# Optimization experiments

Hardware: AMD Instinct MI355X
Metric: run time of the kernel (lower is better)

The kernel has to match this reference:

```python
import jax, jax.numpy as jnp
import numpy as np

B, S, D, H = 2, 2048, 1024, 16
DK = D // H

def setup_inputs() -> dict:
    key = jax.random.key(0)
    k1, k2, k3 = jax.random.split(key, 3)
    std = 2.0 / (D + 3 * D)
    x = jax.random.normal(k1, (B, S, D), dtype=jnp.float32)
    W_qkv = jax.random.normal(k2, (3 * D, D), dtype=jnp.float32) * std
    W_out = jax.random.normal(k3, (D, D), dtype=jnp.float32) * (2.0 / (2 * D))
    return {"x": x, "W_qkv": W_qkv, "W_out": W_out}

def reference(x, W_qkv, W_out):
    # fused QKV projection: [..., d_in] x [d_out, d_in] -> [..., d_out]
    proj = jnp.einsum('bsd,ed->bse', x, W_qkv)               # [B,S,3*H*DK]
    proj = proj.reshape(B, S, 3, H, DK)
    q = proj[:, :, 0].transpose(0, 2, 1, 3)                  # [B,H,S,DK]
    k = proj[:, :, 1].transpose(0, 2, 1, 3)
    v = proj[:, :, 2].transpose(0, 2, 1, 3)
    scores = jnp.einsum('bhnd,bhmd->bhnm', q, k) / jnp.sqrt(jnp.float32(DK))
    causal = jnp.tril(jnp.ones((S, S), dtype=bool))
    scores = jnp.where(causal, scores, -jnp.inf)
    attn = jax.nn.softmax(scores, axis=-1)
    out = jnp.einsum('bhnm,bhmd->bhnd', attn, v)             # [B,H,S,DK]
    out = out.transpose(0, 2, 1, 3).reshape(B, S, H * DK)
    return jnp.einsum('bsd,ed->bse', out, W_out)             # [B,S,D]
```

## Files before the change

kernel.cpp:

```cpp
#include <hip/hip_runtime.h>
#include <hip/hip_bf16.h>
#include <stdint.h>

typedef __attribute__((ext_vector_type(8)))  __bf16 bf16x8;
typedef __attribute__((ext_vector_type(8)))  short  short8;
typedef __attribute__((ext_vector_type(4)))  float  f32x4;
typedef __attribute__((ext_vector_type(16))) float  f32x16;

#define MFMA16(a, b, c) __builtin_amdgcn_mfma_f32_16x16x32_bf16((a), (b), (c), 0, 0, 0)
#define MFMA32(a, b, c) __builtin_amdgcn_mfma_f32_32x32x16_bf16((a), (b), (c), 0, 0, 0)

__device__ __forceinline__ unsigned short f32_bf16(float f) {
  union { float f; unsigned u; } v; v.f = f;
  unsigned r = v.u + 0x7FFFu + ((v.u >> 16) & 1u);
  return (unsigned short)(r >> 16);
}

__device__ __forceinline__ float fast_exp2(float x) {
#if __has_builtin(__builtin_amdgcn_exp2f)
  return __builtin_amdgcn_exp2f(x);
#else
  return __expf(x * 0.69314718f);
#endif
}

__device__ __forceinline__ void gload16(const unsigned short* g, unsigned short* l) {
  __builtin_amdgcn_global_load_lds(
      (const __attribute__((address_space(1))) unsigned int*)(g),
      (__attribute__((address_space(3))) unsigned int*)(l), 16, 0, 0);
}

__global__ void cvt3_kernel(const float* __restrict__ a, int na4,
                            const float* __restrict__ b, int nb4,
                            const float* __restrict__ c, int nc4,
                            unsigned short* __restrict__ oa,
                            unsigned short* __restrict__ ob,
                            unsigned short* __restrict__ oc) {
  int total = na4 + nb4 + nc4;
  for (int i = blockIdx.x * blockDim.x + threadIdx.x; i < total; i += gridDim.x * blockDim.x) {
    const float* src; unsigned short* dst; int j = i;
    if (j < na4) { src = a; dst = oa; }
    else if (j - na4 < nb4) { j -= na4; src = b; dst = ob; }
    else { j -= na4 + nb4; src = c; dst = oc; }
    float4 v = reinterpret_cast<const float4*>(src)[j];
    ushort4 o4;
    o4.x = f32_bf16(v.x); o4.y = f32_bf16(v.y);
    o4.z = f32_bf16(v.z); o4.w = f32_bf16(v.w);
    reinterpret_cast<ushort4*>(dst)[j] = o4;
  }
}

__global__ __launch_bounds__(512, 2) void gemm_qkv_8ph(const unsigned short* __restrict__ A,
                                                       const unsigned short* __restrict__ Bm,
                                                       unsigned short* __restrict__ qkv) {
  extern __shared__ unsigned short SM[];
  const int tid  = threadIdx.x;
  const int lane = tid & 63;
  const int w    = tid >> 6;
  const int wr   = w >> 2, wc = w & 3;
  const int l16  = lane & 15, lh = lane >> 4;
  const int sw   = l16 & 7;
  const int m0   = blockIdx.y * 256;
  const int n0   = blockIdx.x * 256;

  f32x4 acc[8][4];
#pragma unroll
  for (int mi = 0; mi < 8; ++mi)
#pragma unroll
    for (int ni = 0; ni < 4; ++ni) acc[mi][ni] = 0.f;

  const int r0 = tid >> 3,         h0 = (tid & 7) ^ (r0 & 7);
  const int r1 = (tid + 512) >> 3, h1 = (tid & 7) ^ (r1 & 7);
  const unsigned short* Asrc[2][2];
  const unsigned short* Bsrc[2][2];
  Asrc[0][0] = A + (size_t)(m0 + r0) * 1024 + h0 * 8;
  Asrc[0][1] = A + (size_t)(m0 + r1) * 1024 + h1 * 8;
  Asrc[1][0] = A + (size_t)(m0 + 128 + r0) * 1024 + h0 * 8;
  Asrc[1][1] = A + (size_t)(m0 + 128 + r1) * 1024 + h1 * 8;
  Bsrc[0][0] = Bm + (size_t)(n0 + r0) * 1024 + h0 * 8;
  Bsrc[0][1] = Bm + (size_t)(n0 + r1) * 1024 + h1 * 8;
  Bsrc[1][0] = Bm + (size_t)(n0 + 128 + r0) * 1024 + h0 * 8;
  Bsrc[1][1] = Bm + (size_t)(n0 + 128 + r1) * 1024 + h1 * 8;
  const int ld0 = (w * 64) * 8;
  const int ld1 = (512 + w * 64) * 8;

#define STAGE_A(buf, h, U) do { \
    gload16(Asrc[h][0] + (U) * 64, SM + (buf) * 32768 + (h) * 8192 + ld0); \
    gload16(Asrc[h][1] + (U) * 64, SM + (buf) * 32768 + (h) * 8192 + ld1); } while (0)
#define STAGE_B(buf, h, U) do { \
    gload16(Bsrc[h][0] + (U) * 64, SM + (buf) * 32768 + 16384 + (h) * 8192 + ld0); \
    gload16(Bsrc[h][1] + (U) * 64, SM + (buf) * 32768 + 16384 + (h) * 8192 + ld1); } while (0)

  STAGE_A(0, 0, 0); STAGE_A(0, 1, 0);
  STAGE_B(0, 0, 0); STAGE_B(0, 1, 0);
  STAGE_B(1, 0, 1); STAGE_B(1, 1, 1);
  asm volatile("s_waitcnt vmcnt(4)" ::: "memory");
  __builtin_amdgcn_s_barrier();

  const int NT = 16;
#pragma unroll 2
  for (int U = 0; U < NT; ++U) {
    const int b = U & 1;
    const unsigned short* Ab = SM + b * 32768 + wr * 8192;
    const unsigned short* Bb = SM + b * 32768 + 16384 + (wc >> 1) * 8192;
    const int rB = (wc & 1) * 64;
    bf16x8 bfr[4][2], af[2][2];

#define LDA(i, j) (*(const bf16x8*)(Ab + (((i) * 16 + l16) * 8 + (((j) * 4 + lh) ^ sw)) * 8))
#define LDB(n, j) (*(const bf16x8*)(Bb + (((rB + (n) * 16 + l16)) * 8 + (((j) * 4 + lh) ^ sw)) * 8))
#define PHASE_MFMA(p) \
    __builtin_amdgcn_s_setprio(1); \
    _Pragma("unroll") \
    for (int n = 0; n < 4; ++n) { \
      acc[2*(p)][n]   = MFMA16(af[0][0], bfr[n][0], acc[2*(p)][n]); \
      acc[2*(p)][n]   = MFMA16(af[0][1], bfr[n][1], acc[2*(p)][n]); \
      acc[2*(p)+1][n] = MFMA16(af[1][0], bfr[n][0], acc[2*(p)+1][n]); \
      acc[2*(p)+1][n] = MFMA16(af[1][1], bfr[n][1], acc[2*(p)+1][n]); \
    } \
    __builtin_amdgcn_s_setprio(0);

    af[0][0] = LDA(0, 0); af[0][1] = LDA(0, 1);
    af[1][0] = LDA(1, 0); af[1][1] = LDA(1, 1);
#pragma unroll
    for (int n = 0; n < 4; ++n) { bfr[n][0] = LDB(n, 0); bfr[n][1] = LDB(n, 1); }
    if (U + 1 < NT) STAGE_A(b ^ 1, 0, U + 1);
    __builtin_amdgcn_s_barrier();
    PHASE_MFMA(0)
    __builtin_amdgcn_s_barrier();
    af[0][0] = LDA(2, 0); af[0][1] = LDA(2, 1);
    af[1][0] = LDA(3, 0); af[1][1] = LDA(3, 1);
    if (U + 1 < NT) STAGE_A(b ^ 1, 1, U + 1);
    __builtin_amdgcn_s_barrier();
    PHASE_MFMA(1)
    __builtin_amdgcn_s_barrier();
    af[0][0] = LDA(4, 0); af[0][1] = LDA(4, 1);
    af[1][0] = LDA(5, 0); af[1][1] = LDA(5, 1);
    if (U + 2 < NT) STAGE_B(b, 0, U + 2);
    __builtin_amdgcn_s_barrier();
    PHASE_MFMA(2)
    __builtin_amdgcn_s_barrier();
    af[0][0] = LDA(6, 0); af[0][1] = LDA(6, 1);
    af[1][0] = LDA(7, 0); af[1][1] = LDA(7, 1);
    if (U + 2 < NT) STAGE_B(b, 1, U + 2);
    __builtin_amdgcn_s_barrier();
    PHASE_MFMA(3)
    asm volatile("s_waitcnt vmcnt(4)" ::: "memory");
    __builtin_amdgcn_s_barrier();
#undef LDA
#undef LDB
#undef PHASE_MFMA
  }

  __syncthreads();
  unsigned short* Ep = SM + w * 8192;
  const int gn0 = n0 + wc * 64;
  const int cc  = gn0 >> 10;
  const int hh2 = (gn0 & 1023) >> 6;
  const int gm0 = m0 + wr * 128;
  const int bb2 = gm0 >> 11;
  const int ss0 = gm0 & 2047;
  const int bh2 = bb2 * 16 + hh2;

  if (cc < 2) {
    const float qsc = (cc == 0) ? 0.18033688f : 1.0f;
#pragma unroll
    for (int mi = 0; mi < 8; ++mi)
#pragma unroll
      for (int ni = 0; ni < 4; ++ni)
#pragma unroll
        for (int r = 0; r < 4; ++r) {
          int row = mi * 16 + lh * 4 + r;
          int col = (ni * 16 + l16) ^ (lh << 3);
          Ep[row * 64 + col] = f32_bf16(acc[mi][ni][r] * qsc);
        }
    unsigned short* qk = qkv + (((size_t)cc * 32 + bh2) * 2048 + ss0) * 64;
#pragma unroll
    for (int it = 0; it < 16; ++it) {
      int ci = it * 64 + lane;
      int row = ci >> 3, c = ci & 7;
      short8 vv = *(const short8*)(Ep + row * 64 + ((c ^ ((row >> 2) & 3)) * 8));
      *(short8*)(qk + (size_t)row * 64 + c * 8) = vv;
    }
  } else {
#pragma unroll
    for (int mi = 0; mi < 8; ++mi)
#pragma unroll
      for (int ni = 0; ni < 4; ++ni) {
        int dk = ni * 16 + l16;
        int ssl = mi * 16 + lh * 4;
        unsigned lo, hi;
        asm("v_cvt_pk_bf16_f32 %0, %1, %2" : "=v"(lo) : "v"(acc[mi][ni][0]), "v"(acc[mi][ni][1]));
        asm("v_cvt_pk_bf16_f32 %0, %1, %2" : "=v"(hi) : "v"(acc[mi][ni][2]), "v"(acc[mi][ni][3]));
        int off = dk * 128 + (ssl ^ ((dk & 7) << 3));
        *(uint2*)(Ep + off) = make_uint2(lo, hi);
      }
    unsigned short* vt = qkv + (size_t)8388608 + (size_t)bh2 * 64 * 2048 + ss0;
#pragma unroll
    for (int it = 0; it < 16; ++it) {
      int ci = it * 64 + lane;
      int dk = ci >> 4, c = ci & 15;
      short8 vv = *(const short8*)(Ep + dk * 128 + ((c ^ (dk & 7)) * 8));
      *(short8*)(vt + (size_t)dk * 2048 + c * 8) = vv;
    }
  }
#undef STAGE_A
#undef STAGE_B
}

__global__ __launch_bounds__(256) void gemm_out(const unsigned short* __restrict__ A,
                                                const unsigned short* __restrict__ Bm,
                                                float* __restrict__ C,
                                                int M, int N, int K) {
  extern __shared__ unsigned short SM[];
  unsigned short* As = SM;
  unsigned short* Bs = SM + 4096;
  const int tid  = threadIdx.x;
  const int lane = tid & 63;
  const int wid  = tid >> 6;
  const int wr   = wid >> 1, wc = wid & 1;
  const int l16  = lane & 15, lh = lane >> 4;
  const int m0   = blockIdx.y * 128;
  const int n0   = blockIdx.x * 128;

  f32x4 acc[4][4];
#pragma unroll
  for (int mi = 0; mi < 4; ++mi)
#pragma unroll
    for (int ni = 0; ni < 4; ++ni) acc[mi][ni] = 0.f;

  const int c0 = tid, c1 = 256 + tid;
  const unsigned short* a0 = A + (size_t)(m0 + (c0 >> 2)) * K + (c0 & 3) * 8;
  const unsigned short* a1 = A + (size_t)(m0 + (c1 >> 2)) * K + (c1 & 3) * 8;
  const unsigned short* b0 = Bm + (size_t)(n0 + (c0 >> 2)) * K + (c0 & 3) * 8;
  const unsigned short* b1 = Bm + (size_t)(n0 + (c1 >> 2)) * K + (c1 & 3) * 8;
  const int d0 = wid * 64 * 8;
  const int d1 = (256 + wid * 64) * 8;

  for (int k0 = 0; k0 < K; k0 += 32) {
    __syncthreads();
    gload16(a0 + k0, As + d0);
    gload16(a1 + k0, As + d1);
    gload16(b0 + k0, Bs + d0);
    gload16(b1 + k0, Bs + d1);
    __syncthreads();
    bf16x8 af[4], bfr[4];
#pragma unroll
    for (int i = 0; i < 4; ++i) {
      af[i]  = *(const bf16x8*)(As + (wr * 64 + i * 16 + l16) * 32 + lh * 8);
      bfr[i] = *(const bf16x8*)(Bs + (wc * 64 + i * 16 + l16) * 32 + lh * 8);
    }
#pragma unroll
    for (int mi = 0; mi < 4; ++mi)
#pragma unroll
      for (int ni = 0; ni < 4; ++ni)
        acc[mi][ni] = MFMA16(af[mi], bfr[ni], acc[mi][ni]);
  }

  __syncthreads();
  float* Ef = (float*)(SM + wid * 4096);
  const int gm0 = m0 + wr * 64;
  const int gn0 = n0 + wc * 64;
#pragma unroll
  for (int p = 0; p < 2; ++p) {
#pragma unroll
    for (int mi = 0; mi < 4; ++mi)
#pragma unroll
      for (int q = 0; q < 2; ++q) {
        int ni = 2 * p + q;
#pragma unroll
        for (int r = 0; r < 4; ++r) {
          int row = mi * 16 + lh * 4 + r;
          int col = (q * 16 + l16) ^ ((row & 7) << 2);
          Ef[row * 32 + col] = acc[mi][ni][r];
        }
      }
#pragma unroll
    for (int it = 0; it < 8; ++it) {
      int ci = it * 64 + lane;
      int row = ci >> 3, c4 = ci & 7;
      float4 vv = *(const float4*)(Ef + row * 32 + ((c4 * 4) ^ ((row & 7) << 2)));
      *(float4*)(&C[(size_t)(gm0 + row) * N + gn0 + p * 32 + c4 * 4]) = vv;
    }
  }
}

__device__ const signed char JQT[48] = {31,31,30,15, 30,29,29,28,14, 28,27,27,26,13, 26,25,25,24,12,
                                        24,23,23,22,11, 22,21,21,20,10, 20,19,19,18, 9, 18,17,17,16, 8,
                                        16, 7, 6, 5, 4, 3, 2, 1, 0};
__device__ const signed char JS0[48] = { 0,16, 0, 0, 16, 0,15, 0, 0, 15, 0,14, 0, 0, 14, 0,13, 0, 0,
                                        13, 0,12, 0, 0, 12, 0,11, 0, 0, 11, 0,10, 0, 0, 10, 0, 9, 0, 0,
                                         9, 0, 0, 0, 0, 0, 0, 0, 0};
__device__ const signed char JNT[48] = {16,16,16,16, 15,15,15,15,15, 14,14,14,14,14, 13,13,13,13,13,
                                        12,12,12,12,12, 11,11,11,11,11, 10,10,10,10,10,  9, 9, 9, 9, 9,
                                         8, 8, 7, 6, 5, 4, 3, 2, 1};
__device__ const signed char JSL[48] = {30,31,28,-1, 29,26,27,24,-1, 25,22,23,20,-1, 21,18,19,16,-1,
                                        17,14,15,12,-1, 13,10,11, 8,-1,  9, 6, 7, 4,-1,  5, 2, 3, 0,-1,
                                         1,-1,-1,-1,-1,-1,-1,-1,-1};

__global__ __launch_bounds__(256) void attn_kernel(const unsigned short* __restrict__ Qg,
                                                   const unsigned short* __restrict__ Kg,
                                                   const unsigned short* __restrict__ Vtg,
                                                   unsigned short* __restrict__ Og,
                                                   char* __restrict__ parts) {
  __shared__ unsigned short Ks[2][64 * 64];
  __shared__ unsigned short Vs[2][64 * 64];

  const int tid  = threadIdx.x;
  const int lane = tid & 63;
  const int w    = tid >> 6;
  const int wq   = w & 1, wkv = w >> 1;
  const int l31  = lane & 31, hi = lane >> 5;
  const int rx0  = (l31 ^ (l31 >> 3)) & 7;

  const int jb   = blockIdx.x >> 5;
  const int bh   = blockIdx.x & 31;
  const int qt   = JQT[jb];
  const int ts0  = JS0[jb];
  const int tend = ts0 + JNT[jb];
  const int slot = JSL[jb];
  const int bb   = bh >> 4, hh = bh & 15;
  const int qb   = qt * 64;
  const int qcol = qb + wq * 32 + l31;

  const unsigned short* Qh = Qg + (size_t)bh * (2048 * 64);
  const unsigned short* Kh = Kg + (size_t)bh * (2048 * 64);
  const unsigned short* Vh = Vtg + (size_t)bh * (64 * 2048);

  bf16x8 qf[4];
#pragma unroll
  for (int ks = 0; ks < 4; ++ks)
    qf[ks] = *(const bf16x8*)(Qh + (size_t)qcol * 64 + ks * 16 + hi * 8);

  f32x16 o0 = 0.f, o1 = 0.f;
  float mreg = 0.f, ll = 0.f;

  const int sA = tid, sB = tid + 256;
  const int rA = sA >> 3, hA = (sA & 7) ^ ((rA ^ (rA >> 3)) & 7);
  const int rB = sB >> 3, hB = (sB & 7) ^ ((rB ^ (rB >> 3)) & 7);
  const unsigned short* kSrcA = Kh + rA * 64 + hA * 8;
  const unsigned short* kSrcB = Kh + rB * 64 + hB * 8;
  const unsigned short* vSrcA = Vh + (size_t)rA * 2048 + hA * 8;
  const unsigned short* vSrcB = Vh + (size_t)rB * 2048 + hB * 8;
  const int ldsA = (w * 64) * 8;
  const int ldsB = (256 + w * 64) * 8;

  gload16(kSrcA + (size_t)(ts0 * 64) * 64, &Ks[0][ldsA]);
  gload16(kSrcB + (size_t)(ts0 * 64) * 64, &Ks[0][ldsB]);
  gload16(vSrcA + ts0 * 64, &Vs[0][ldsA]);
  gload16(vSrcB + ts0 * 64, &Vs[0][ldsB]);
  __syncthreads();

  const unsigned short* kA = kSrcA + (size_t)(ts0 + 1) * 4096;
  const unsigned short* kB = kSrcB + (size_t)(ts0 + 1) * 4096;
  const unsigned short* vA = vSrcA + (ts0 + 1) * 64;
  const unsigned short* vB = vSrcB + (ts0 + 1) * 64;

  for (int t = ts0; t < tend; ++t) {
    const int kv0 = t * 64;
    const int cur = (t - ts0) & 1;
    if (t + 1 < tend) {
      gload16(kA, &Ks[cur ^ 1][ldsA]);
      gload16(kB, &Ks[cur ^ 1][ldsB]);
      gload16(vA, &Vs[cur ^ 1][ldsA]);
      gload16(vB, &Vs[cur ^ 1][ldsB]);
      kA += 4096; kB += 4096; vA += 64; vB += 64;
    }
    const unsigned short* Kb = Ks[cur];
    const unsigned short* Vb = Vs[cur];

    f32x16 s = 0.f;
    const int kvl = wkv * 32 + l31;
#pragma unroll
    for (int ks = 0; ks < 4; ++ks) {
      int c = (ks * 2 + hi) ^ rx0 ^ (wkv << 2);
      bf16x8 ka = *(const bf16x8*)(Kb + kvl * 64 + c * 8);
      s = MFMA32(ka, qf[ks], s);
    }

    if (t == qt) {
#pragma unroll
      for (int r = 0; r < 16; ++r) {
        int kvp = kv0 + wkv * 32 + (r & 3) + 8 * (r >> 2) + 4 * hi;
        if (kvp > qcol) s[r] = -__builtin_inff();
      }
    }

    float pm = fmaxf(fmaxf(s[0], s[1]), s[2]);
    pm = fmaxf(fmaxf(pm, s[3]), s[4]);
    pm = fmaxf(fmaxf(pm, s[5]), s[6]);
    pm = fmaxf(fmaxf(pm, s[7]), s[8]);
    pm = fmaxf(fmaxf(pm, s[9]), s[10]);
    pm = fmaxf(fmaxf(pm, s[11]), s[12]);
    pm = fmaxf(fmaxf(pm, s[13]), s[14]);
    pm = fmaxf(pm, s[15]);
    if (!__all(pm <= mreg + 8.f)) {
      float t0 = fmaxf(pm, __shfl_xor(pm, 32));
      float mn = fmaxf(mreg, t0);
      float esc = fast_exp2(mreg - mn);
      mreg = mn; ll *= esc;
#pragma unroll
      for (int r = 0; r < 16; ++r) { o0[r] *= esc; o1[r] *= esc; }
    }

    float p[16];
#pragma unroll
    for (int r = 0; r < 16; ++r) p[r] = fast_exp2(s[r] - mreg);
    float ps = ((p[0] + p[1]) + (p[2] + p[3])) + ((p[4] + p[5]) + (p[6] + p[7]))
             + ((p[8] + p[9]) + (p[10] + p[11])) + ((p[12] + p[13]) + (p[14] + p[15]));
    ps += __shfl_xor(ps, 32);
    ll += ps;

    bf16x8 pf[2];
#pragma unroll
    for (int ks = 0; ks < 2; ++ks) {
      const int off = ks * 8;
      unsigned a1, b1, a2, b2;
      asm("v_cvt_pk_bf16_f32 %0, %1, %2" : "=v"(a1) : "v"(p[off + 0]), "v"(p[off + 1]));
      asm("v_cvt_pk_bf16_f32 %0, %1, %2" : "=v"(b1) : "v"(p[off + 4]), "v"(p[off + 5]));
      asm("v_cvt_pk_bf16_f32 %0, %1, %2" : "=v"(a2) : "v"(p[off + 2]), "v"(p[off + 3]));
      asm("v_cvt_pk_bf16_f32 %0, %1, %2" : "=v"(b2) : "v"(p[off + 6]), "v"(p[off + 7]));
      asm("v_permlane32_swap_b32 %0, %1" : "+v"(a1), "+v"(b1));
      asm("v_permlane32_swap_b32 %0, %1" : "+v"(a2), "+v"(b2));
      union { unsigned u[4]; bf16x8 f; } fr;
      fr.u[0] = a1; fr.u[1] = a2; fr.u[2] = b1; fr.u[3] = b2;
      pf[ks] = fr.f;
    }

#pragma unroll
    for (int ks = 0; ks < 2; ++ks) {
      int cbase = wkv * 4 + ks * 2 + hi;
      bf16x8 va0 = *(const bf16x8*)(Vb + l31 * 64 + (cbase ^ rx0) * 8);
      bf16x8 va1 = *(const bf16x8*)(Vb + (32 + l31) * 64 + (cbase ^ rx0 ^ 4) * 8);
      o0 = MFMA32(va0, pf[ks], o0);
      o1 = MFMA32(va1, pf[ks], o1);
    }
    __syncthreads();
  }

  float* oxch = (float*)Ks;
  float* lmx  = (float*)Vs;
  if (wkv == 1) {
    float* dst = oxch + wq * 2048;
#pragma unroll
    for (int r = 0; r < 16; ++r) {
      int d0 = (r & 3) + 8 * (r >> 2) + 4 * hi;
      dst[d0 * 32 + l31] = o0[r];
      dst[(32 + d0) * 32 + l31] = o1[r];
    }
    if (hi == 0) { lmx[wq * 64 + l31] = ll; lmx[wq * 64 + 32 + l31] = mreg; }
  }
  __syncthreads();
  if (wkv == 0) {
    float lB = lmx[wq * 64 + l31];
    float mB = lmx[wq * 64 + 32 + l31];
    float mx = fmaxf(mreg, mB);
    float wA = fast_exp2(mreg - mx), wB = fast_exp2(mB - mx);
    float lT = ll * wA + lB * wB;
    float inv = (slot < 0) ? (1.f / lT) : 1.f;
    float sA2 = wA * inv, sB2 = wB * inv;
    const float* src = oxch + wq * 2048;
    unsigned short* slab = (unsigned short*)((char*)Vs + 1024) + wq * 2048;
#pragma unroll
    for (int i = 0; i < 8; ++i) {
      int r = 2 * i;
      int d0 = (r & 3) + 8 * (r >> 2) + 4 * hi;
      float x0 = o0[r] * sA2 + src[d0 * 32 + l31] * sB2;
      float x1 = o0[r + 1] * sA2 + src[(d0 + 1) * 32 + l31] * sB2;
      float y0 = o1[r] * sA2 + src[(32 + d0) * 32 + l31] * sB2;
      float y1 = o1[r + 1] * sA2 + src[(33 + d0) * 32 + l31] * sB2;
      unsigned u0, u1;
      asm("v_cvt_pk_bf16_f32 %0, %1, %2" : "=v"(u0) : "v"(x0), "v"(x1));
      asm("v_cvt_pk_bf16_f32 %0, %1, %2" : "=v"(u1) : "v"(y0), "v"(y1));
      *(unsigned*)(slab + l31 * 64 + (((d0 >> 3) ^ (l31 & 7)) * 8) + (d0 & 7)) = u0;
      int d1 = 32 + d0;
      *(unsigned*)(slab + l31 * 64 + (((d1 >> 3) ^ (l31 & 7)) * 8) + (d1 & 7)) = u1;
    }
    if (slot < 0) {
      unsigned short* op = Og + (size_t)bb * 2048 * 1024 + (size_t)hh * 64;
#pragma unroll
      for (int it = 0; it < 4; ++it) {
        int ci = it * 64 + lane;
        int qr = ci >> 3, c = ci & 7;
        short8 vv = *(const short8*)(slab + qr * 64 + ((c ^ (qr & 7)) * 8));
        *(short8*)(op + (size_t)(qb + wq * 32 + qr) * 1024 + c * 8) = vv;
      }
    } else {
      char* pb = parts + (size_t)(bh * 32 + slot) * 8704;
      float* pl = (float*)pb;
      float* pmv = pl + 64;
      unsigned short* pO = (unsigned short*)(pb + 512);
      if (hi == 0) { pl[wq * 32 + l31] = lT; pmv[wq * 32 + l31] = mx; }
#pragma unroll
      for (int it = 0; it < 4; ++it) {
        int ci = it * 64 + lane;
        int qr = ci >> 3, c = ci & 7;
        short8 vv = *(const short8*)(slab + qr * 64 + ((c ^ (qr & 7)) * 8));
        *(short8*)(pO + (size_t)(wq * 32 + qr) * 64 + c * 8) = vv;
      }
    }
  }
}

__global__ __launch_bounds__(256) void merge_kernel(const char* __restrict__ parts,
                                                    unsigned short* __restrict__ Og) {
  const int task = blockIdx.x;
  const int bh = task & 31, qi = task >> 5;
  const int qt = 16 + qi;
  const int bb = bh >> 4, hh = bh & 15;
  const int tid = threadIdx.x;
  const int r = tid >> 2, q = tid & 3;

  const char* pb1 = parts + (size_t)(bh * 32 + 2 * qi) * 8704;
  const char* pb2 = parts + (size_t)(bh * 32 + 2 * qi + 1) * 8704;
  const float* l1p = (const float*)pb1;
  const float* l2p = (const float*)pb2;
  float lv1 = l1p[r], mv1 = l1p[64 + r];
  float lv2 = l2p[r], mv2 = l2p[64 + r];
  float mx = fmaxf(mv1, mv2);
  float w1 = fast_exp2(mv1 - mx), w2 = fast_exp2(mv2 - mx);
  float inv = 1.f / (lv1 * w1 + lv2 * w2);
  float s1 = w1 * inv, s2 = w2 * inv;

  const unsigned short* O1 = (const unsigned short*)(pb1 + 512) + r * 64 + q * 16;
  const unsigned short* O2 = (const unsigned short*)(pb2 + 512) + r * 64 + q * 16;
  short8 a0 = *(const short8*)(O1);
  short8 a1 = *(const short8*)(O1 + 8);
  short8 b0 = *(const short8*)(O2);
  short8 b1 = *(const short8*)(O2 + 8);

  unsigned outw[8];
#pragma unroll
  for (int i = 0; i < 4; ++i) {
    float x0 = __builtin_bit_cast(float, ((unsigned)(unsigned short)a0[2 * i]) << 16) * s1 +
               __builtin_bit_cast(float, ((unsigned)(unsigned short)b0[2 * i]) << 16) * s2;
    float x1 = __builtin_bit_cast(float, ((unsigned)(unsigned short)a0[2 * i + 1]) << 16) * s1 +
               __builtin_bit_cast(float, ((unsigned)(unsigned short)b0[2 * i + 1]) << 16) * s2;
    asm("v_cvt_pk_bf16_f32 %0, %1, %2" : "=v"(outw[i]) : "v"(x0), "v"(x1));
    float y0 = __builtin_bit_cast(float, ((unsigned)(unsigned short)a1[2 * i]) << 16) * s1 +
               __builtin_bit_cast(float, ((unsigned)(unsigned short)b1[2 * i]) << 16) * s2;
    float y1 = __builtin_bit_cast(float, ((unsigned)(unsigned short)a1[2 * i + 1]) << 16) * s1 +
               __builtin_bit_cast(float, ((unsigned)(unsigned short)b1[2 * i + 1]) << 16) * s2;
    asm("v_cvt_pk_bf16_f32 %0, %1, %2" : "=v"(outw[4 + i]) : "v"(y0), "v"(y1));
  }
  unsigned short* op = Og + ((size_t)bb * 2048 + qt * 64 + r) * 1024 + hh * 64 + q * 16;
  *(uint4*)(op)     = make_uint4(outw[0], outw[1], outw[2], outw[3]);
  *(uint4*)(op + 8) = make_uint4(outw[4], outw[5], outw[6], outw[7]);
}

extern "C" void kernel_launch(void* const* d_in, const int* in_sizes, int n_in,
                              void* d_out, int out_size, void* d_ws, size_t ws_size,
                              hipStream_t stream) {
  const float* x    = (const float*)d_in[0];
  const float* Wqkv = (const float*)d_in[1];
  const float* Wout = (const float*)d_in[2];
  float* out = (float*)d_out;

  char* ws = (char*)d_ws;
  unsigned short* xb  = (unsigned short*)(ws);
  unsigned short* wqb = (unsigned short*)(ws + (size_t)8 * 1024 * 1024);
  unsigned short* wob = (unsigned short*)(ws + (size_t)14 * 1024 * 1024);
  unsigned short* qkv = (unsigned short*)(ws + (size_t)16 * 1024 * 1024);
  unsigned short* att = (unsigned short*)(ws + (size_t)40 * 1024 * 1024);
  char* parts = ws;

  static bool attr_set = false;
  if (!attr_set) {
    hipFuncSetAttribute((const void*)gemm_qkv_8ph,
                        hipFuncAttributeMaxDynamicSharedMemorySize, 131072);
    attr_set = true;
  }

  cvt3_kernel<<<2048, 256, 0, stream>>>(x, 4194304 / 4, Wqkv, 3145728 / 4,
                                        Wout, 1048576 / 4, xb, wqb, wob);

  gemm_qkv_8ph<<<dim3(12, 16), 512, 131072, stream>>>(xb, wqb, qkv);

  const unsigned short* Qp  = qkv;
  const unsigned short* Kp  = qkv + 4194304;
  const unsigned short* Vtp = qkv + 8388608;
  attn_kernel<<<1536, 256, 0, stream>>>(Qp, Kp, Vtp, att, parts);
  merge_kernel<<<512, 256, 0, stream>>>(parts, att);

  gemm_out<<<dim3(8, 32), 256, 32768, stream>>>(att, wob, out, 4096, 1024, 1024);
}
```

Before: 112.5 us.

## Shrink output GEMM tile to 64x128 and compute softmax row sums via MFMA

The output projection GEMM now uses 64x128 tiles with each wave owning a 64x32 slice, doubling the grid to 512 blocks to fill more CUs at the cost of lower per-block operand reuse. In the attention kernel, the per-row softmax denominator is no longer built from scalar adds plus a cross-lane shuffle. It is accumulated by two extra MFMAs that multiply an all-ones matrix by the bf16 probability fragments, so the sum is taken over bf16-rounded probabilities and adds matrix-core work in exchange for fewer VALU ops.

```diff
diff --git a/kernel.cpp b/kernel.cpp
--- a/kernel.cpp
+++ b/kernel.cpp
@@ -213,74 +213,65 @@
                                                 int M, int N, int K) {
   extern __shared__ unsigned short SM[];
   unsigned short* As = SM;
-  unsigned short* Bs = SM + 4096;
+  unsigned short* Bs = SM + 2048;
   const int tid  = threadIdx.x;
   const int lane = tid & 63;
   const int wid  = tid >> 6;
-  const int wr   = wid >> 1, wc = wid & 1;
   const int l16  = lane & 15, lh = lane >> 4;
-  const int m0   = blockIdx.y * 128;
+  const int m0   = blockIdx.y * 64;
   const int n0   = blockIdx.x * 128;
 
-  f32x4 acc[4][4];
+  f32x4 acc[4][2];
 #pragma unroll
   for (int mi = 0; mi < 4; ++mi)
 #pragma unroll
-    for (int ni = 0; ni < 4; ++ni) acc[mi][ni] = 0.f;
-
-  const int c0 = tid, c1 = 256 + tid;
-  const unsigned short* a0 = A + (size_t)(m0 + (c0 >> 2)) * K + (c0 & 3) * 8;
-  const unsigned short* a1 = A + (size_t)(m0 + (c1 >> 2)) * K + (c1 & 3) * 8;
-  const unsigned short* b0 = Bm + (size_t)(n0 + (c0 >> 2)) * K + (c0 & 3) * 8;
-  const unsigned short* b1 = Bm + (size_t)(n0 + (c1 >> 2)) * K + (c1 & 3) * 8;
-  const int d0 = wid * 64 * 8;
-  const int d1 = (256 + wid * 64) * 8;
+    for (int ni = 0; ni < 2; ++ni) acc[mi][ni] = 0.f;
+
+  const unsigned short* aSrc = A + (size_t)(m0 + (tid >> 2)) * K + (tid & 3) * 8;
+  const unsigned short* b0   = Bm + (size_t)(n0 + (tid >> 2)) * K + (tid & 3) * 8;
+  const unsigned short* b1   = Bm + (size_t)(n0 + 64 + (tid >> 2)) * K + (tid & 3) * 8;
+  const int dA  = wid * 512;
+  const int dB0 = wid * 512;
+  const int dB1 = 2048 + wid * 512;
 
   for (int k0 = 0; k0 < K; k0 += 32) {
     __syncthreads();
-    gload16(a0 + k0, As + d0);
-    gload16(a1 + k0, As + d1);
-    gload16(b0 + k0, Bs + d0);
-    gload16(b1 + k0, Bs + d1);
+    gload16(aSrc + k0, As + dA);
+    gload16(b0 + k0, Bs + dB0);
+    gload16(b1 + k0, Bs + dB1);
     __syncthreads();
-    bf16x8 af[4], bfr[4];
-#pragma unroll
-    for (int i = 0; i < 4; ++i) {
-      af[i]  = *(const bf16x8*)(As + (wr * 64 + i * 16 + l16) * 32 + lh * 8);
-      bfr[i] = *(const bf16x8*)(Bs + (wc * 64 + i * 16 + l16) * 32 + lh * 8);
-    }
+    bf16x8 af[4], bfr[2];
 #pragma unroll
     for (int mi = 0; mi < 4; ++mi)
-#pragma unroll
-      for (int ni = 0; ni < 4; ++ni)
+      af[mi] = *(const bf16x8*)(As + (mi * 16 + l16) * 32 + lh * 8);
+#pragma unroll
+    for (int ni = 0; ni < 2; ++ni)
+      bfr[ni] = *(const bf16x8*)(Bs + (wid * 32 + ni * 16 + l16) * 32 + lh * 8);
+#pragma unroll
+    for (int mi = 0; mi < 4; ++mi)
+#pragma unroll
+      for (int ni = 0; ni < 2; ++ni)
         acc[mi][ni] = MFMA16(af[mi], bfr[ni], acc[mi][ni]);
   }
 
   __syncthreads();
-  float* Ef = (float*)(SM + wid * 4096);
-  const int gm0 = m0 + wr * 64;
-  const int gn0 = n0 + wc * 64;
-#pragma unroll
-  for (int p = 0; p < 2; ++p) {
-#pragma unroll
-    for (int mi = 0; mi < 4; ++mi)
-#pragma unroll
-      for (int q = 0; q < 2; ++q) {
-        int ni = 2 * p + q;
-#pragma unroll
-        for (int r = 0; r < 4; ++r) {
-          int row = mi * 16 + lh * 4 + r;
-          int col = (q * 16 + l16) ^ ((row & 7) << 2);
-          Ef[row * 32 + col] = acc[mi][ni][r];
-        }
+  float* Ef = (float*)SM + wid * 2048;
+#pragma unroll
+  for (int mi = 0; mi < 4; ++mi)
+#pragma unroll
+    for (int ni = 0; ni < 2; ++ni)
+#pragma unroll
+      for (int r = 0; r < 4; ++r) {
+        int row = mi * 16 + lh * 4 + r;
+        int col = (ni * 16 + l16) ^ ((row & 7) << 2);
+        Ef[row * 32 + col] = acc[mi][ni][r];
       }
 #pragma unroll
-    for (int it = 0; it < 8; ++it) {
-      int ci = it * 64 + lane;
-      int row = ci >> 3, c4 = ci & 7;
-      float4 vv = *(const float4*)(Ef + row * 32 + ((c4 * 4) ^ ((row & 7) << 2)));
-      *(float4*)(&C[(size_t)(gm0 + row) * N + gn0 + p * 32 + c4 * 4]) = vv;
-    }
+  for (int it = 0; it < 8; ++it) {
+    int ci = it * 64 + lane;
+    int row = ci >> 3, c4 = ci & 7;
+    float4 vv = *(const float4*)(Ef + row * 32 + ((c4 * 4) ^ ((row & 7) << 2)));
+    *(float4*)(&C[(size_t)(m0 + row) * N + n0 + wid * 32 + c4 * 4]) = vv;
   }
 }
 
@@ -331,8 +322,14 @@
   for (int ks = 0; ks < 4; ++ks)
     qf[ks] = *(const bf16x8*)(Qh + (size_t)qcol * 64 + ks * 16 + hi * 8);
 
+  union { short8 s; bf16x8 b; } oneu;
+#pragma unroll
+  for (int j = 0; j < 8; ++j) oneu.s[j] = 0x3F80;
+  const bf16x8 onesf = oneu.b;
+
   f32x16 o0 = 0.f, o1 = 0.f;
-  float mreg = 0.f, ll = 0.f;
+  f32x16 o_l = 0.f;
+  float mreg = 0.f;
 
   const int sA = tid, sB = tid + 256;
   const int rA = sA >> 3, hA = (sA & 7) ^ ((rA ^ (rA >> 3)) & 7);
@@ -397,7 +394,8 @@
       float t0 = fmaxf(pm, __shfl_xor(pm, 32));
       float mn = fmaxf(mreg, t0);
       float esc = fast_exp2(mreg - mn);
-      mreg = mn; ll *= esc;
+      mreg = mn;
+      o_l[0] *= esc;
 #pragma unroll
       for (int r = 0; r < 16; ++r) { o0[r] *= esc; o1[r] *= esc; }
     }
@@ -405,10 +403,6 @@
     float p[16];
 #pragma unroll
     for (int r = 0; r < 16; ++r) p[r] = fast_exp2(s[r] - mreg);
-    float ps = ((p[0] + p[1]) + (p[2] + p[3])) + ((p[4] + p[5]) + (p[6] + p[7]))
-             + ((p[8] + p[9]) + (p[10] + p[11])) + ((p[12] + p[13]) + (p[14] + p[15]));
-    ps += __shfl_xor(ps, 32);
-    ll += ps;
 
     bf16x8 pf[2];
 #pragma unroll
@@ -426,6 +420,9 @@
       pf[ks] = fr.f;
     }
 
+    o_l = MFMA32(onesf, pf[0], o_l);
+    o_l = MFMA32(onesf, pf[1], o_l);
+
 #pragma unroll
     for (int ks = 0; ks < 2; ++ks) {
       int cbase = wkv * 4 + ks * 2 + hi;
@@ -436,6 +433,8 @@
     }
     __syncthreads();
   }
+
+  const float ll = o_l[0];
 
   float* oxch = (float*)Ks;
   float* lmx  = (float*)Vs;
@@ -581,5 +580,5 @@
   attn_kernel<<<1536, 256, 0, stream>>>(Qp, Kp, Vtp, att, parts);
   merge_kernel<<<512, 256, 0, stream>>>(parts, att);
 
-  gemm_out<<<dim3(8, 32), 256, 32768, stream>>>(att, wob, out, 4096, 1024, 1024);
-}
+  gemm_out<<<dim3(8, 64), 256, 32768, stream>>>(att, wob, out, 4096, 1024, 1024);
+}
```

Result: no change. 113.2 us (+0.6%).
